# Performance work log

Measured on AMD Instinct MI355X. Metric: run time of the kernel, lower is better.

The kernel has to match this reference:

```python
import jax, jax.numpy as jnp
import numpy as np

B, T, U, D, V = 8, 128, 64, 512, 1024

def setup_inputs() -> dict:
    key = jax.random.key(0)
    k1, k2, k3, k4, k5, k6 = jax.random.split(key, 6)
    source_encodings = jax.random.normal(k1, (B, T, D), dtype=jnp.float32)
    target_encodings = jax.random.normal(k2, (B, U, D), dtype=jnp.float32)
    source_lengths = jax.random.randint(k3, (B,), 1, T + 1, dtype=jnp.int32)
    target_lengths = jax.random.randint(k4, (B,), 1, U + 1, dtype=jnp.int32)
    # Linear(D, V): weight (V, D), bias (V), init like torch default (uniform)
    bound = 1.0 / np.sqrt(D)
    W = jax.random.uniform(k5, (V, D), minval=-bound, maxval=bound, dtype=jnp.float32)
    b = jax.random.uniform(k6, (V,), minval=-bound, maxval=bound, dtype=jnp.float32)
    return {"source_encodings": source_encodings, "source_lengths": source_lengths,
            "target_encodings": target_encodings, "target_lengths": target_lengths,
            "W": W, "b": b}

def reference(source_encodings, source_lengths, target_encodings, target_lengths, W, b):
    # broadcast add: (B,T,1,D) + (B,1,U,D) -> (B,T,U,D)
    joint = source_encodings[:, :, None, :] + target_encodings[:, None, :, :]
    relu_out = jax.nn.relu(joint)
    # linear projection: (B,T,U,D) x (D,V) + b -> (B,T,U,V)
    output = jnp.einsum('btud,vd->btuv', relu_out, W) + b
    return (output, source_lengths, target_lengths)
```

## Files before the change

kernel.cpp:

```cpp
#include <hip/hip_runtime.h>

typedef unsigned short u16;
typedef float  f32x4  __attribute__((ext_vector_type(4)));
typedef int    i32x4  __attribute__((ext_vector_type(4)));
typedef __bf16 bf16x8 __attribute__((ext_vector_type(8)));

constexpr int B_ = 8, T_ = 128, U_ = 64, D_ = 512, V_ = 1024;
constexpr int M_ = B_ * T_ * U_;

__global__ void prep_w(const float* __restrict__ W,
                       const int* __restrict__ sl, const int* __restrict__ tl,
                       u16* __restrict__ Wb2, float* __restrict__ tail) {
  if (blockIdx.x == 0 && threadIdx.x < 16) {
    const int t = threadIdx.x;
    tail[t] = (t < 8) ? (float)sl[t] : (float)tl[t - 8];
  }
  const int tid = blockIdx.x * 256 + threadIdx.x;
  const int v  = tid >> 6;
  const int cs = tid & 63;
  const float* sp = W + (size_t)v * D_ + cs * 8;
  float4 w0 = *(const float4*)sp;
  float4 w1 = *(const float4*)(sp + 4);
  union { __bf16 h[8]; i32x4 x; } pk;
  pk.h[0] = (__bf16)w0.x; pk.h[1] = (__bf16)w0.y;
  pk.h[2] = (__bf16)w0.z; pk.h[3] = (__bf16)w0.w;
  pk.h[4] = (__bf16)w1.x; pk.h[5] = (__bf16)w1.y;
  pk.h[6] = (__bf16)w1.z; pk.h[7] = (__bf16)w1.w;
  const int vg = v >> 4, vc = v & 15;
  const int kc = cs >> 2, ko = cs & 3;
  *(i32x4*)(Wb2 + (((size_t)(vg * 16 + kc) * 64 + ko * 16 + vc) * 8)) = pk.x;
}

__global__ void tail_k(const int* __restrict__ sl, const int* __restrict__ tl,
                       float* __restrict__ tail) {
  const int t = threadIdx.x;
  if (t < 8)       tail[t] = (float)sl[t];
  else if (t < 16) tail[t] = (float)tl[t - 8];
}

__global__ __launch_bounds__(256, 3) void joiner_gemm(
    const float* __restrict__ src, const float* __restrict__ tgt,
    const u16* __restrict__ Wb2, const float* __restrict__ bias,
    float* __restrict__ out)
{
  __shared__ __align__(16) char As[2][16384];

  const int tid  = threadIdx.x;
  const int lane = tid & 63;
  const int wid  = tid >> 6;
  const int bn   = blockIdx.x & 7;
  const int bm   = blockIdx.x >> 3;
  const int bt0  = bm * 2;
  const int bb   = bt0 >> 7;
  const int sr0  = tid >> 3;
  const int sc8  = tid & 7;
  const int wm   = (wid >> 1) * 64;
  const int wn   = (wid & 1) * 64;

  f32x4 acc[4][4] = {};

  const float* srcp0 = src + (size_t)bt0 * D_ + sc8 * 8;
  const float* srcp1 = srcp0 + D_;
  const float* tgtp0 = tgt + ((size_t)bb * U_ + sr0) * D_ + sc8 * 8;
  const float* tgtp1 = tgtp0 + (size_t)32 * D_;

  float bv[4];
  #pragma unroll
  for (int ni = 0; ni < 4; ++ni)
    bv[ni] = bias[bn * 128 + wn + ni * 16 + (lane & 15)];

  const u16* bfr[4];
  #pragma unroll
  for (int ni = 0; ni < 4; ++ni) {
    const int vg = bn * 8 + (wn >> 4) + ni;
    bfr[ni] = Wb2 + ((size_t)vg * 16 * 64 + lane) * 8;
  }

  float4 pS0a, pS0b, pS1a, pS1b, pT0a, pT0b, pT1a, pT1b;
  bf16x8 bg[4][2];

  auto loadA = [&](int kt) {
    const int k0 = kt * 64;
    pS0a = *(const float4*)(srcp0 + k0); pS0b = *(const float4*)(srcp0 + k0 + 4);
    pS1a = *(const float4*)(srcp1 + k0); pS1b = *(const float4*)(srcp1 + k0 + 4);
    pT0a = *(const float4*)(tgtp0 + k0); pT0b = *(const float4*)(tgtp0 + k0 + 4);
    pT1a = *(const float4*)(tgtp1 + k0); pT1b = *(const float4*)(tgtp1 + k0 + 4);
  };

  auto loadBg = [&](int kt) {
    #pragma unroll
    for (int ni = 0; ni < 4; ++ni)
      #pragma unroll
      for (int s = 0; s < 2; ++s)
        bg[ni][s] = *(const bf16x8*)(bfr[ni] + (size_t)(kt * 2 + s) * 512);
  };

  auto expandA = [&](int nb) {
    #pragma unroll
    for (int i = 0; i < 2; ++i) {
      const float4 sa = i ? pS1a : pS0a;
      const float4 sb = i ? pS1b : pS0b;
      #pragma unroll
      for (int j = 0; j < 2; ++j) {
        const float4 ta = j ? pT1a : pT0a;
        const float4 tb = j ? pT1b : pT0b;
        const int r = i * 64 + j * 32 + sr0;
        union { __bf16 h[8]; i32x4 x; } pk;
        pk.h[0] = (__bf16)fmaxf(sa.x + ta.x, 0.f);
        pk.h[1] = (__bf16)fmaxf(sa.y + ta.y, 0.f);
        pk.h[2] = (__bf16)fmaxf(sa.z + ta.z, 0.f);
        pk.h[3] = (__bf16)fmaxf(sa.w + ta.w, 0.f);
        pk.h[4] = (__bf16)fmaxf(sb.x + tb.x, 0.f);
        pk.h[5] = (__bf16)fmaxf(sb.y + tb.y, 0.f);
        pk.h[6] = (__bf16)fmaxf(sb.z + tb.z, 0.f);
        pk.h[7] = (__bf16)fmaxf(sb.w + tb.w, 0.f);
        *(i32x4*)(As[nb] + r * 128 + ((sc8 ^ (r & 7)) << 4)) = pk.x;
      }
    }
  };

  auto compute = [&](int cb) {
    #pragma unroll
    for (int s = 0; s < 2; ++s) {
      const int kc = s * 4 + (lane >> 4);
      bf16x8 af[4];
      #pragma unroll
      for (int mi = 0; mi < 4; ++mi) {
        const int r = wm + mi * 16 + (lane & 15);
        af[mi] = *(const bf16x8*)(As[cb] + r * 128 + ((kc ^ (r & 7)) << 4));
      }
      #pragma unroll
      for (int mi = 0; mi < 4; ++mi)
        #pragma unroll
        for (int ni = 0; ni < 4; ++ni)
          acc[mi][ni] = __builtin_amdgcn_mfma_f32_16x16x32_bf16(
              af[mi], bg[ni][s], acc[mi][ni], 0, 0, 0);
    }
  };

  loadA(0);
  expandA(0);
  loadBg(0);
  asm volatile("s_waitcnt lgkmcnt(0)" ::: "memory");
  __builtin_amdgcn_sched_barrier(0);
  __builtin_amdgcn_s_barrier();
  __builtin_amdgcn_sched_barrier(0);

  for (int kt = 0; kt < 8; ++kt) {
    if (kt < 7) loadA(kt + 1);
    __builtin_amdgcn_sched_barrier(0);
    compute(kt & 1);
    if (kt < 7) {
      __builtin_amdgcn_sched_barrier(0);
      loadBg(kt + 1);
      expandA((kt + 1) & 1);
      asm volatile("s_waitcnt lgkmcnt(0)" ::: "memory");
      __builtin_amdgcn_sched_barrier(0);
      __builtin_amdgcn_s_barrier();
      __builtin_amdgcn_sched_barrier(0);
    }
  }

  const int col = lane & 15;
  const int r4  = (lane >> 4) * 4;
  #pragma unroll
  for (int mi = 0; mi < 4; ++mi) {
    const size_t mrow = (size_t)bm * 128 + wm + mi * 16 + r4;
    float* op0 = out + mrow * V_ + bn * 128 + wn + col;
    #pragma unroll
    for (int ni = 0; ni < 4; ++ni) {
      float* op = op0 + ni * 16;
      const f32x4 v = acc[mi][ni];
      op[0 * V_] = v[0] + bv[ni];
      op[1 * V_] = v[1] + bv[ni];
      op[2 * V_] = v[2] + bv[ni];
      op[3 * V_] = v[3] + bv[ni];
    }
  }
}

__global__ __launch_bounds__(256, 2) void joiner_gemm_f32(
    const float* __restrict__ src, const float* __restrict__ tgt,
    const float* __restrict__ Wf, const float* __restrict__ bias,
    float* __restrict__ out)
{
  __shared__ char As[128 * 128];
  __shared__ char Bs[128 * 128];

  const int tid  = threadIdx.x;
  const int lane = tid & 63;
  const int wid  = tid >> 6;
  const int bn   = blockIdx.x & 7;
  const int bm   = blockIdx.x >> 3;
  const int bt0  = bm * 2;
  const int bb   = bt0 >> 7;
  const int sr0  = tid >> 3;
  const int sc8  = tid & 7;
  const int wm   = (wid >> 1) * 64;
  const int wn   = (wid & 1) * 64;

  f32x4 acc[4][4] = {};

  const float* srcp0 = src + (size_t)bt0 * D_ + sc8 * 8;
  const float* srcp1 = srcp0 + D_;
  const float* tgtp0 = tgt + ((size_t)bb * U_ + sr0) * D_ + sc8 * 8;
  const float* tgtp1 = tgtp0 + (size_t)32 * D_;

  for (int kt = 0; kt < 8; ++kt) {
    const int k0 = kt * 64;
    #pragma unroll
    for (int jj = 0; jj < 4; ++jj) {
      const int vr = sr0 + 32 * jj;
      const float* wp = Wf + (size_t)(bn * 128 + vr) * D_ + k0 + sc8 * 8;
      float4 w0 = *(const float4*)wp;
      float4 w1 = *(const float4*)(wp + 4);
      union { __bf16 h[8]; i32x4 x; } pk;
      pk.h[0] = (__bf16)w0.x; pk.h[1] = (__bf16)w0.y;
      pk.h[2] = (__bf16)w0.z; pk.h[3] = (__bf16)w0.w;
      pk.h[4] = (__bf16)w1.x; pk.h[5] = (__bf16)w1.y;
      pk.h[6] = (__bf16)w1.z; pk.h[7] = (__bf16)w1.w;
      *(i32x4*)(Bs + vr * 128 + ((sc8 ^ (vr & 7)) << 4)) = pk.x;
    }
    float4 s0a = *(const float4*)(srcp0 + k0), s0b = *(const float4*)(srcp0 + k0 + 4);
    float4 s1a = *(const float4*)(srcp1 + k0), s1b = *(const float4*)(srcp1 + k0 + 4);
    float4 t0a = *(const float4*)(tgtp0 + k0), t0b = *(const float4*)(tgtp0 + k0 + 4);
    float4 t1a = *(const float4*)(tgtp1 + k0), t1b = *(const float4*)(tgtp1 + k0 + 4);
    #pragma unroll
    for (int i = 0; i < 2; ++i) {
      const float4 sa = i ? s1a : s0a;
      const float4 sb = i ? s1b : s0b;
      #pragma unroll
      for (int jj = 0; jj < 2; ++jj) {
        const float4 ta = jj ? t1a : t0a;
        const float4 tb = jj ? t1b : t0b;
        const int r = i * 64 + jj * 32 + sr0;
        union { __bf16 h[8]; i32x4 x; } pk;
        pk.h[0] = (__bf16)fmaxf(sa.x + ta.x, 0.f);
        pk.h[1] = (__bf16)fmaxf(sa.y + ta.y, 0.f);
        pk.h[2] = (__bf16)fmaxf(sa.z + ta.z, 0.f);
        pk.h[3] = (__bf16)fmaxf(sa.w + ta.w, 0.f);
        pk.h[4] = (__bf16)fmaxf(sb.x + tb.x, 0.f);
        pk.h[5] = (__bf16)fmaxf(sb.y + tb.y, 0.f);
        pk.h[6] = (__bf16)fmaxf(sb.z + tb.z, 0.f);
        pk.h[7] = (__bf16)fmaxf(sb.w + tb.w, 0.f);
        *(i32x4*)(As + r * 128 + ((sc8 ^ (r & 7)) << 4)) = pk.x;
      }
    }
    __syncthreads();
    #pragma unroll
    for (int s = 0; s < 2; ++s) {
      const int kc = s * 4 + (lane >> 4);
      bf16x8 af[4], bg[4];
      #pragma unroll
      for (int mi = 0; mi < 4; ++mi) {
        const int r = wm + mi * 16 + (lane & 15);
        af[mi] = *(const bf16x8*)(As + r * 128 + ((kc ^ (r & 7)) << 4));
      }
      #pragma unroll
      for (int ni = 0; ni < 4; ++ni) {
        const int n = wn + ni * 16 + (lane & 15);
        bg[ni] = *(const bf16x8*)(Bs + n * 128 + ((kc ^ (n & 7)) << 4));
      }
      #pragma unroll
      for (int mi = 0; mi < 4; ++mi)
        #pragma unroll
        for (int ni = 0; ni < 4; ++ni)
          acc[mi][ni] = __builtin_amdgcn_mfma_f32_16x16x32_bf16(
              af[mi], bg[ni], acc[mi][ni], 0, 0, 0);
    }
    __syncthreads();
  }

  const int col = lane & 15;
  const int r4  = (lane >> 4) * 4;
  float bv[4];
  #pragma unroll
  for (int ni = 0; ni < 4; ++ni) bv[ni] = bias[bn * 128 + wn + ni * 16 + col];
  #pragma unroll
  for (int mi = 0; mi < 4; ++mi) {
    const size_t mrow = (size_t)bm * 128 + wm + mi * 16 + r4;
    float* op0 = out + mrow * V_ + bn * 128 + wn + col;
    #pragma unroll
    for (int ni = 0; ni < 4; ++ni) {
      float* op = op0 + ni * 16;
      const f32x4 v = acc[mi][ni];
      op[0 * V_] = v[0] + bv[ni];
      op[1 * V_] = v[1] + bv[ni];
      op[2 * V_] = v[2] + bv[ni];
      op[3 * V_] = v[3] + bv[ni];
    }
  }
}

extern "C" void kernel_launch(void* const* d_in, const int* in_sizes, int n_in,
                              void* d_out, int out_size, void* d_ws, size_t ws_size,
                              hipStream_t stream) {
  const float* src  = (const float*)d_in[0];
  const int*   sl   = (const int*)d_in[1];
  const float* tgt  = (const float*)d_in[2];
  const int*   tl   = (const int*)d_in[3];
  const float* W    = (const float*)d_in[4];
  const float* bias = (const float*)d_in[5];
  float* out  = (float*)d_out;
  float* tail = out + (size_t)M_ * V_;

  if (ws_size >= (size_t)V_ * D_ * sizeof(u16)) {
    u16* Wb2 = (u16*)d_ws;
    prep_w<<<256, 256, 0, stream>>>(W, sl, tl, Wb2, tail);
    joiner_gemm<<<(M_ / 128) * (V_ / 128), 256, 0, stream>>>(
        src, tgt, Wb2, bias, out);
  } else {
    tail_k<<<1, 64, 0, stream>>>(sl, tl, tail);
    joiner_gemm_f32<<<(M_ / 128) * (V_ / 128), 256, 0, stream>>>(
        src, tgt, W, bias, out);
  }
}
```

Baseline: 103.0 us.

## Drop register prefetch of A and B tiles to raise occupancy to four blocks

Removes the software register prefetch: the src/tgt loads for the next k-tile and the bf16 weight fragments are no longer held in registers across the compute phase. Weights are now loaded from global memory inside compute right before the MFMAs, and A loads happen directly in expandA. This frees VGPRs so launch_bounds can be raised from 3 to 4 blocks per CU. The cost is that global load latency is exposed inside the MFMA loop and after each compute, with more resident waves expected to hide it.

After: 108.2 us. 5.0% more time.

```diff
diff --git a/kernel.cpp b/kernel.cpp
--- a/kernel.cpp
+++ b/kernel.cpp
@@ -38,7 +38,7 @@
   else if (t < 16) tail[t] = (float)tl[t - 8];
 }
 
-__global__ __launch_bounds__(256, 3) void joiner_gemm(
+__global__ __launch_bounds__(256, 4) void joiner_gemm(
     const float* __restrict__ src, const float* __restrict__ tgt,
     const u16* __restrict__ Wb2, const float* __restrict__ bias,
     float* __restrict__ out)
@@ -69,41 +69,26 @@
   for (int ni = 0; ni < 4; ++ni)
     bv[ni] = bias[bn * 128 + wn + ni * 16 + (lane & 15)];
 
-  const u16* bfr[4];
-  #pragma unroll
-  for (int ni = 0; ni < 4; ++ni) {
-    const int vg = bn * 8 + (wn >> 4) + ni;
-    bfr[ni] = Wb2 + ((size_t)vg * 16 * 64 + lane) * 8;
-  }
-
-  float4 pS0a, pS0b, pS1a, pS1b, pT0a, pT0b, pT1a, pT1b;
-  bf16x8 bg[4][2];
-
-  auto loadA = [&](int kt) {
+  const u16* bbase = Wb2 + ((size_t)(bn * 8 + (wn >> 4)) * 16 * 64 + lane) * 8;
+
+  auto expandA = [&](int kt, int nb) {
     const int k0 = kt * 64;
-    pS0a = *(const float4*)(srcp0 + k0); pS0b = *(const float4*)(srcp0 + k0 + 4);
-    pS1a = *(const float4*)(srcp1 + k0); pS1b = *(const float4*)(srcp1 + k0 + 4);
-    pT0a = *(const float4*)(tgtp0 + k0); pT0b = *(const float4*)(tgtp0 + k0 + 4);
-    pT1a = *(const float4*)(tgtp1 + k0); pT1b = *(const float4*)(tgtp1 + k0 + 4);
-  };
-
-  auto loadBg = [&](int kt) {
-    #pragma unroll
-    for (int ni = 0; ni < 4; ++ni)
-      #pragma unroll
-      for (int s = 0; s < 2; ++s)
-        bg[ni][s] = *(const bf16x8*)(bfr[ni] + (size_t)(kt * 2 + s) * 512);
-  };
-
-  auto expandA = [&](int nb) {
+    const float4 s0a = *(const float4*)(srcp0 + k0);
+    const float4 s0b = *(const float4*)(srcp0 + k0 + 4);
+    const float4 s1a = *(const float4*)(srcp1 + k0);
+    const float4 s1b = *(const float4*)(srcp1 + k0 + 4);
+    const float4 t0a = *(const float4*)(tgtp0 + k0);
+    const float4 t0b = *(const float4*)(tgtp0 + k0 + 4);
+    const float4 t1a = *(const float4*)(tgtp1 + k0);
+    const float4 t1b = *(const float4*)(tgtp1 + k0 + 4);
     #pragma unroll
     for (int i = 0; i < 2; ++i) {
-      const float4 sa = i ? pS1a : pS0a;
-      const float4 sb = i ? pS1b : pS0b;
+      const float4 sa = i ? s1a : s0a;
+      const float4 sb = i ? s1b : s0b;
       #pragma unroll
       for (int j = 0; j < 2; ++j) {
-        const float4 ta = j ? pT1a : pT0a;
-        const float4 tb = j ? pT1b : pT0b;
+        const float4 ta = j ? t1a : t0a;
+        const float4 tb = j ? t1b : t0b;
         const int r = i * 64 + j * 32 + sr0;
         union { __bf16 h[8]; i32x4 x; } pk;
         pk.h[0] = (__bf16)fmaxf(sa.x + ta.x, 0.f);
@@ -119,9 +104,14 @@
     }
   };
 
-  auto compute = [&](int cb) {
+  auto compute = [&](int kt, int cb) {
     #pragma unroll
     for (int s = 0; s < 2; ++s) {
+      bf16x8 bgs[4];
+      #pragma unroll
+      for (int ni = 0; ni < 4; ++ni)
+        bgs[ni] = *(const bf16x8*)(bbase + (size_t)ni * 8192
+                                         + (size_t)(kt * 2 + s) * 512);
       const int kc = s * 4 + (lane >> 4);
       bf16x8 af[4];
       #pragma unroll
@@ -134,26 +124,21 @@
         #pragma unroll
         for (int ni = 0; ni < 4; ++ni)
           acc[mi][ni] = __builtin_amdgcn_mfma_f32_16x16x32_bf16(
-              af[mi], bg[ni][s], acc[mi][ni], 0, 0, 0);
+              af[mi], bgs[ni], acc[mi][ni], 0, 0, 0);
     }
   };
 
-  loadA(0);
-  expandA(0);
-  loadBg(0);
+  expandA(0, 0);
   asm volatile("s_waitcnt lgkmcnt(0)" ::: "memory");
   __builtin_amdgcn_sched_barrier(0);
   __builtin_amdgcn_s_barrier();
   __builtin_amdgcn_sched_barrier(0);
 
   for (int kt = 0; kt < 8; ++kt) {
-    if (kt < 7) loadA(kt + 1);
-    __builtin_amdgcn_sched_barrier(0);
-    compute(kt & 1);
+    compute(kt, kt & 1);
     if (kt < 7) {
       __builtin_amdgcn_sched_barrier(0);
-      loadBg(kt + 1);
-      expandA((kt + 1) & 1);
+      expandA(kt + 1, (kt + 1) & 1);
       asm volatile("s_waitcnt lgkmcnt(0)" ::: "memory");
       __builtin_amdgcn_sched_barrier(0);
       __builtin_amdgcn_s_barrier();
```
